# Performance work log

Measured on AMD Instinct MI355X. Metric: run time of the kernel, lower is better.

The kernel has to match this reference:

```python
import jax, jax.numpy as jnp
import numpy as np

B, N, E = 64, 512, 8192          # graphs, nodes per graph, edges per graph
F_IN, H, C = 128, 128, 10        # in features, hidden, classes
K1, K2 = 256, 128                # dense pool cluster counts: ceil(.5*N), ceil(.5*K1)
EPS = 1e-15


def setup_inputs():
    key = jax.random.key(0)
    keys = jax.random.split(key, 32)
    it = iter(keys)
    def w(shape, fan_in):
        return jax.random.normal(next(it), shape, jnp.float32) / np.sqrt(fan_in)
    x = jax.random.normal(next(it), (B * N, F_IN), jnp.float32)
    src_l = jax.random.randint(next(it), (B, E), 0, N)
    dst_l = jax.random.randint(next(it), (B, E), 0, N)
    off = (jnp.arange(B) * N)[:, None]
    src = (src_l + off).reshape(-1).astype(jnp.int32)
    dst = (dst_l + off).reshape(-1).astype(jnp.int32)
    return dict(
        x=x, src=src, dst=dst,
        conv0_wr=w((F_IN, H), F_IN), conv0_wroot=w((F_IN, H), F_IN), conv0_b=jnp.zeros((H,), jnp.float32),
        sconv2_wr=w((H, H), H), sconv2_wroot=w((H, H), H), sconv2_b=jnp.zeros((H,), jnp.float32),
        sconv3_wr=w((H, H), H), sconv3_wroot=w((H, H), H), sconv3_b=jnp.zeros((H,), jnp.float32),
        sage1_wr=w((H, H), H), sage1_wroot=w((H, H), H), sage1_b=jnp.zeros((H,), jnp.float32),
        sage2_wr=w((H, H), H), sage2_wroot=w((H, H), H), sage2_b=jnp.zeros((H,), jnp.float32),
        pool0_w=w((H, K1), H), pool0_b=jnp.zeros((K1,), jnp.float32),
        pool1_w=w((H, K2), H), pool1_b=jnp.zeros((K2,), jnp.float32),
        p1=w((H,), H), p2=w((H,), H), p3=w((H,), H),
        lin1_1_w=w((2 * H, H), 2 * H), lin1_1_b=jnp.zeros((H,), jnp.float32),
        lin1_w=w((H, H), H), lin1_b=jnp.zeros((H,), jnp.float32),
        lin2_w=w((2 * H, C), 2 * H), lin2_b=jnp.zeros((C,), jnp.float32),
    )


def _graph_conv(x, src, dst, emask, wr, wroot, b, n):
    # PyG GraphConv: lin_rel(sum_j x_j) + lin_root(x_i); invalid edges masked to 0.
    msg = x[src] * emask[:, None]
    agg = jax.ops.segment_sum(msg, dst, num_segments=n)
    return agg @ wr + x @ wroot + b


def _topk_pool(x, score_w, src, dst, emask, n_per_graph, k):
    # TopK pooling (MPoolS): score = x.w/||w||, keep top ratio*n per graph, gate by tanh(score).
    score = x @ score_w / (jnp.linalg.norm(score_w) + 1e-16)
    idx = jax.lax.top_k(score.reshape(B, n_per_graph), k)[1]
    perm = (idx + (jnp.arange(B) * n_per_graph)[:, None]).reshape(-1)
    new_x = x[perm] * jnp.tanh(score[perm])[:, None]
    new_id = jnp.full((B * n_per_graph,), -1, jnp.int32).at[perm].set(
        jnp.arange(B * k, dtype=jnp.int32))
    ns, nd = new_id[src], new_id[dst]
    valid = (ns >= 0) & (nd >= 0) & (emask > 0)
    return new_x, jnp.where(valid, ns, 0), jnp.where(valid, nd, 0), valid.astype(x.dtype)


def _readout(x, k):
    # gmp || gap per graph (nodes are contiguous, k per graph)
    xr = x.reshape(B, k, -1)
    return jnp.concatenate([xr.max(axis=1), xr.mean(axis=1)], axis=-1)


def _dense_sage(x, adj, wr, wroot, b):
    agg = (adj @ x) / jnp.clip(adj.sum(-1, keepdims=True), 1.0, None)
    return agg @ wr + x @ wroot + b


def _dense_mincut_pool(x, adj, s):
    s = jax.nn.softmax(s, axis=-1)
    k = s.shape[-1]
    out = jnp.einsum('bnk,bnf->bkf', s, x)
    out_adj = jnp.einsum('bnk,bnm,bml->bkl', s, adj, s)
    mincut_num = jnp.trace(out_adj, axis1=-2, axis2=-1)
    deg = adj.sum(-1)
    mincut_den = jnp.einsum('bn,bnk,bnk->b', deg, s, s)
    mc = -jnp.mean(mincut_num / (mincut_den + EPS))
    ss = jnp.einsum('bnk,bnl->bkl', s, s)
    ss_n = jnp.linalg.norm(ss, axis=(1, 2), keepdims=True)
    eye = jnp.eye(k, dtype=x.dtype)
    o = jnp.mean(jnp.linalg.norm(ss / (ss_n + EPS) - eye / jnp.sqrt(k), axis=(1, 2)))
    di = jnp.arange(k)
    out_adj = out_adj.at[:, di, di].set(0.0)
    dpool = jnp.sqrt(out_adj.sum(-1)) + EPS
    out_adj = out_adj / dpool[:, :, None] / dpool[:, None, :]
    return out, out_adj, mc, o


def _forward(x, src, dst, conv0_wr, conv0_wroot, conv0_b, sconv2_wr, sconv2_wroot, sconv2_b,
             sconv3_wr, sconv3_wroot, sconv3_b, sage1_wr, sage1_wroot, sage1_b,
             sage2_wr, sage2_wroot, sage2_b, pool0_w, pool0_b, pool1_w, pool1_b,
             p1, p2, p3, lin1_1_w, lin1_1_b, lin1_w, lin1_b, lin2_w, lin2_b):
    relu = jax.nn.relu
    e0 = jnp.ones((src.shape[0],), x.dtype)
    x0 = relu(_graph_conv(x, src, dst, e0, conv0_wr, conv0_wroot, conv0_b, B * N))
    # ---- sparse (MPoolS / top-k) branch, stage 1 ----
    sx, s1, d1, m1 = _topk_pool(x0, p1, src, dst, e0, N, N // 2)
    sx1 = _readout(sx, N // 2)
    # ---- dense (DiffPool-style) branch ----
    xd = x0.reshape(B, N, H)                               # to_dense_batch (full mask)
    g = src // N
    adj = jnp.zeros((B, N, N), x.dtype).at[g, src % N, dst % N].add(1.0)  # to_dense_adj
    s = xd @ pool0_w + pool0_b
    xd, adj, mc, o = _dense_mincut_pool(xd, adj, s)
    xd = relu(_dense_sage(xd, adj, sage1_wr, sage1_wroot, sage1_b))
    s = xd @ pool1_w + pool1_b
    xd, adj, mc2, o2 = _dense_mincut_pool(xd, adj, s)
    mc, o = mc + mc2, o + o2
    xd = _dense_sage(xd, adj, sage2_wr, sage2_wroot, sage2_b)
    xg = relu(xd.mean(axis=1) @ lin1_w + lin1_b)
    # ---- sparse branch, stages 2 and 3 ----
    sx = relu(_graph_conv(sx, s1, d1, m1, sconv2_wr, sconv2_wroot, sconv2_b, B * (N // 2)))
    sx, s2, d2, m2 = _topk_pool(sx, p2, s1, d1, m1, N // 2, N // 4)
    sx2 = _readout(sx, N // 4)
    sx = relu(_graph_conv(sx, s2, d2, m2, sconv3_wr, sconv3_wroot, sconv3_b, B * (N // 4)))
    sx, s3, d3, m3 = _topk_pool(sx, p3, s2, d2, m2, N // 4, N // 8)
    sx3 = _readout(sx, N // 8)
    sxr = relu((sx1 + sx2 + sx3) @ lin1_1_w + lin1_1_b)
    logits = jnp.concatenate([sxr, xg], axis=-1) @ lin2_w + lin2_b
    return logits, mc, o


def reference(x, src, dst, conv0_wr, conv0_wroot, conv0_b, sconv2_wr, sconv2_wroot, sconv2_b,
              sconv3_wr, sconv3_wroot, sconv3_b, sage1_wr, sage1_wroot, sage1_b,
              sage2_wr, sage2_wroot, sage2_b, pool0_w, pool0_b, pool1_w, pool1_b,
              p1, p2, p3, lin1_1_w, lin1_1_b, lin1_w, lin1_b, lin2_w, lin2_b):
    return _forward(x, src, dst, conv0_wr, conv0_wroot, conv0_b, sconv2_wr, sconv2_wroot,
                    sconv2_b, sconv3_wr, sconv3_wroot, sconv3_b, sage1_wr, sage1_wroot,
                    sage1_b, sage2_wr, sage2_wroot, sage2_b, pool0_w, pool0_b, pool1_w,
                    pool1_b, p1, p2, p3, lin1_1_w, lin1_1_b, lin1_w, lin1_b, lin2_w, lin2_b)
```

## Files before the change

kernel.cpp:

```cpp
#include <hip/hip_runtime.h>
#include <math.h>

#define NGRAPH 64
#define NE 524288
#define EPG 8192
#define TSZ 2560

typedef short s16x8 __attribute__((ext_vector_type(8)));
typedef float f32x4 __attribute__((ext_vector_type(4)));

__device__ inline unsigned short f2bf(float f) {
    unsigned int u = __float_as_uint(f);
    return (unsigned short)((u + 0x7FFFu + ((u >> 16) & 1u)) >> 16);
}

__global__ void edge_count(const int* __restrict__ key, const float* __restrict__ mask,
                           int* __restrict__ counts) {
    int e = blockIdx.x * 256 + threadIdx.x;
    if (e < NE && (!mask || mask[e] > 0.f)) atomicAdd(&counts[key[e]], 1);
}

__global__ __launch_bounds__(512) void scan_offsets(const int* __restrict__ counts,
        int* __restrict__ offs, int* __restrict__ cursor, int nPerGraph) {
    __shared__ int s[512];
    const int g = blockIdx.x, t = threadIdx.x;
    int v = (t < nPerGraph) ? counts[g * nPerGraph + t] : 0;
    s[t] = v; __syncthreads();
    for (int d = 1; d < 512; d <<= 1) {
        int u = (t >= d) ? s[t - d] : 0;
        __syncthreads();
        s[t] += u;
        __syncthreads();
    }
    if (t < nPerGraph) {
        int o = g * EPG + s[t] - v;
        offs[g * nPerGraph + t] = o;
        cursor[g * nPerGraph + t] = o;
    }
}

__global__ void edge_fill(const int* __restrict__ key, const int* __restrict__ payload,
                          const float* __restrict__ mask, int* __restrict__ cursor,
                          int* __restrict__ elist) {
    int e = blockIdx.x * 256 + threadIdx.x;
    if (e < NE && (!mask || mask[e] > 0.f)) {
        int p = atomicAdd(&cursor[key[e]], 1);
        elist[p] = payload[e];
    }
}

__global__ __launch_bounds__(256) void gather_csr(
    const float* __restrict__ xfeat, int Fx,
    const int* __restrict__ offs, const int* __restrict__ cnts,
    const int* __restrict__ elist,
    float* __restrict__ out, int totRows, int rowsPerGraph)
{
    const int gid = (blockIdx.x * 256 + threadIdx.x) >> 5;
    const int lane = threadIdx.x & 31;
    const int csh = (Fx == 256) ? 1 : 0;
    const int rid = gid >> csh;
    const int c0 = (gid & ((1 << csh) - 1)) << 7;
    if (rid >= totRows) return;
    const int row = (rid & 63) * rowsPerGraph + (rid >> 6);
    const int beg = offs[row];
    const int n = cnts[row];
    const long long co = (long long)c0 + (lane << 2);
    float4 acc = make_float4(0.f, 0.f, 0.f, 0.f);
    int j = 0;
    for (; j + 4 <= n; j += 4) {
        const int n0 = elist[beg + j], n1 = elist[beg + j + 1];
        const int n2 = elist[beg + j + 2], n3 = elist[beg + j + 3];
        const float4 v0 = *(const float4*)&xfeat[(long long)n0 * Fx + co];
        const float4 v1 = *(const float4*)&xfeat[(long long)n1 * Fx + co];
        const float4 v2 = *(const float4*)&xfeat[(long long)n2 * Fx + co];
        const float4 v3 = *(const float4*)&xfeat[(long long)n3 * Fx + co];
        acc.x += v0.x + v1.x + v2.x + v3.x;
        acc.y += v0.y + v1.y + v2.y + v3.y;
        acc.z += v0.z + v1.z + v2.z + v3.z;
        acc.w += v0.w + v1.w + v2.w + v3.w;
    }
    for (; j < n; ++j) {
        const float4 v = *(const float4*)&xfeat[(long long)elist[beg + j] * Fx + co];
        acc.x += v.x; acc.y += v.y; acc.z += v.z; acc.w += v.w;
    }
    *(float4*)&out[(long long)row * Fx + co] = acc;
}

__global__ void i2f(const int* __restrict__ a, float* __restrict__ b, int n) {
    int i = blockIdx.x * 256 + threadIdx.x;
    if (i < n) b[i] = (float)a[i];
}

__global__ void wconv2_t(const float* __restrict__ W1, const float* __restrict__ W2,
                         int K1, int K2, int Nn,
                         unsigned short* __restrict__ outh, unsigned short* __restrict__ outl) {
    int idx = blockIdx.x * 256 + threadIdx.x;
    int Kt = K1 + K2;
    if (idx >= Nn * Kt) return;
    int n = idx / Kt, k = idx - n * Kt;
    float v = (k < K1) ? W1[(long long)k * Nn + n] : W2[(long long)(k - K1) * Nn + n];
    unsigned short h = f2bf(v);
    float hf = __uint_as_float((unsigned int)h << 16);
    outh[idx] = h;
    outl[idx] = f2bf(v - hf);
}

__device__ inline void stageN_split(const float* __restrict__ src, int ldk, int k0,
                                    short* lds, int tid, const float* __restrict__ rs, int m0) {
    const int r = tid >> 2, kq = (tid & 3) << 3;
    const float* p = src + (long long)r * ldk + k0 + kq;
    float v[8];
    *(float4*)v = *(const float4*)p;
    *(float4*)(v + 4) = *(const float4*)(p + 4);
    if (rs) { float s = rs[m0 + r]; for (int i = 0; i < 8; ++i) v[i] *= s; }
    s16x8 hv, lv;
    #pragma unroll
    for (int i = 0; i < 8; ++i) {
        unsigned short h = f2bf(v[i]);
        float hf = __uint_as_float((unsigned int)h << 16);
        hv[i] = (short)h;
        lv[i] = (short)f2bf(v[i] - hf);
    }
    *(s16x8*)(lds + r * 40 + kq) = hv;
    *(s16x8*)(lds + TSZ + r * 40 + kq) = lv;
}

__device__ inline void stageT_split(const float* __restrict__ src, int ldm, int k0, int m0,
                                    short* lds, int tid) {
    const int kp = tid >> 4, mc = tid & 15;
    const int k = kp << 1;
    const float* p0 = src + (long long)(k0 + k) * ldm + m0 + mc;
    const float* p1 = p0 + ldm;
    #pragma unroll
    for (int i = 0; i < 4; ++i) {
        float a = p0[i << 4], b = p1[i << 4];
        unsigned short ha = f2bf(a), hb = f2bf(b);
        float hfa = __uint_as_float((unsigned int)ha << 16);
        float hfb = __uint_as_float((unsigned int)hb << 16);
        unsigned short la = f2bf(a - hfa), lb = f2bf(b - hfb);
        const int o = (mc + (i << 4)) * 40 + k;
        *(unsigned int*)(lds + o) = (unsigned int)ha | ((unsigned int)hb << 16);
        *(unsigned int*)(lds + o + TSZ) = (unsigned int)la | ((unsigned int)lb << 16);
    }
}

__device__ inline void stageW_split(const unsigned short* __restrict__ wh,
                                    const unsigned short* __restrict__ wl, int ldk,
                                    int n0, int k0, short* lds, int tid) {
    const int r = tid >> 2, kq = (tid & 3) << 3;
    *(s16x8*)(lds + r * 40 + kq) = *(const s16x8*)(wh + (long long)(n0 + r) * ldk + k0 + kq);
    *(s16x8*)(lds + TSZ + r * 40 + kq) = *(const s16x8*)(wl + (long long)(n0 + r) * ldk + k0 + kq);
}

__device__ inline void mfma_split(const short* As, const short* Bs, int wm, int wn,
                                  int l15, int quad, f32x4 (&acc)[2][2]) {
    const int ko = quad << 3;
    s16x8 ah[2], al[2], bh[2], bl[2];
    #pragma unroll
    for (int i = 0; i < 2; ++i) {
        const int ra = (wm + (i << 4) + l15) * 40 + ko;
        const int rb = (wn + (i << 4) + l15) * 40 + ko;
        ah[i] = *(const s16x8*)&As[ra];
        al[i] = *(const s16x8*)&As[TSZ + ra];
        bh[i] = *(const s16x8*)&Bs[rb];
        bl[i] = *(const s16x8*)&Bs[TSZ + rb];
    }
    #pragma unroll
    for (int mi = 0; mi < 2; ++mi)
    #pragma unroll
    for (int ni = 0; ni < 2; ++ni) {
        f32x4 c = acc[mi][ni];
        c = __builtin_amdgcn_mfma_f32_16x16x32_bf16(ah[mi], bh[ni], c, 0, 0, 0);
        c = __builtin_amdgcn_mfma_f32_16x16x32_bf16(ah[mi], bl[ni], c, 0, 0, 0);
        c = __builtin_amdgcn_mfma_f32_16x16x32_bf16(al[mi], bh[ni], c, 0, 0, 0);
        acc[mi][ni] = c;
    }
}

__global__ __launch_bounds__(256) void gemm_aw(
    const float* __restrict__ A1, int K1, const float* __restrict__ A2, int K2,
    const float* __restrict__ rscale,
    const unsigned short* __restrict__ Wh, const unsigned short* __restrict__ Wl,
    const float* __restrict__ bias, float* __restrict__ C, int Nn, int doRelu)
{
    __shared__ short As[2 * TSZ], Bs[2 * TSZ];
    const int m0 = blockIdx.y << 6, n0 = blockIdx.x << 6;
    const int tid = threadIdx.x, lane = tid & 63, wv = tid >> 6;
    const int l15 = lane & 15, quad = lane >> 4;
    const int wm = (wv & 1) << 5, wn = (wv >> 1) << 5;
    f32x4 acc[2][2] = {};
    const int Kt = K1 + K2;
    for (int k0 = 0; k0 < Kt; k0 += 32) {
        if (k0 < K1) stageN_split(A1 + (long long)m0 * K1, K1, k0, As, tid, rscale, m0);
        else         stageN_split(A2 + (long long)m0 * K2, K2, k0 - K1, As, tid, nullptr, 0);
        stageW_split(Wh, Wl, Kt, n0, k0, Bs, tid);
        __syncthreads();
        mfma_split(As, Bs, wm, wn, l15, quad, acc);
        __syncthreads();
    }
    #pragma unroll
    for (int mi = 0; mi < 2; ++mi)
    #pragma unroll
    for (int ni = 0; ni < 2; ++ni) {
        const int col = n0 + wn + (ni << 4) + l15;
        const float bv = bias ? bias[col] : 0.f;
        #pragma unroll
        for (int r = 0; r < 4; ++r) {
            const int row = m0 + wm + (mi << 4) + (quad << 2) + r;
            float v = acc[mi][ni][r] + bv;
            if (doRelu) v = fmaxf(v, 0.f);
            C[(long long)row * Nn + col] = v;
        }
    }
}

__global__ __launch_bounds__(256) void gemm_tt(
    const float* __restrict__ At, const float* __restrict__ Bkn,
    float* __restrict__ C, float* __restrict__ fro,
    int Kd, int Mm, int Nn, int dual,
    long long sA, long long sB, long long sC)
{
    __shared__ short As[2 * TSZ], Bs[2 * TSZ], A2s[2 * TSZ];
    __shared__ float redf[4];
    const int z = blockIdx.x;
    const float* Ap = At + (long long)z * sA;
    const float* Bp = Bkn + (long long)z * sB;
    const int m0 = blockIdx.y << 6, n0 = blockIdx.z << 6;
    const int tid = threadIdx.x, lane = tid & 63, wv = tid >> 6;
    const int l15 = lane & 15, quad = lane >> 4;
    const int wm = (wv & 1) << 5, wn = (wv >> 1) << 5;
    f32x4 acc[2][2] = {};
    f32x4 accA[2][2] = {};
    for (int k0 = 0; k0 < Kd; k0 += 32) {
        stageT_split(Ap, Mm, k0, m0, As, tid);
        stageT_split(Bp, Nn, k0, n0, Bs, tid);
        if (dual) stageT_split(Ap, Mm, k0, n0, A2s, tid);
        __syncthreads();
        mfma_split(As, Bs, wm, wn, l15, quad, acc);
        if (dual) mfma_split(As, A2s, wm, wn, l15, quad, accA);
        __syncthreads();
    }
    float* Cp = C + (long long)z * sC;
    #pragma unroll
    for (int mi = 0; mi < 2; ++mi)
    #pragma unroll
    for (int ni = 0; ni < 2; ++ni) {
        const int col = n0 + wn + (ni << 4) + l15;
        #pragma unroll
        for (int r = 0; r < 4; ++r) {
            const int row = m0 + wm + (mi << 4) + (quad << 2) + r;
            Cp[(long long)row * Nn + col] = acc[mi][ni][r];
        }
    }
    if (dual) {
        float s = 0.f;
        #pragma unroll
        for (int mi = 0; mi < 2; ++mi)
        #pragma unroll
        for (int ni = 0; ni < 2; ++ni)
        #pragma unroll
        for (int r = 0; r < 4; ++r) s += accA[mi][ni][r] * accA[mi][ni][r];
        for (int off = 32; off; off >>= 1) s += __shfl_xor(s, off);
        if (lane == 0) redf[wv] = s;
        __syncthreads();
        if (tid == 0) atomicAdd(&fro[z], redf[0] + redf[1] + redf[2] + redf[3]);
    }
}

__global__ __launch_bounds__(256) void gemm_nt(
    const float* __restrict__ A, const float* __restrict__ Bkn, float* __restrict__ C,
    int Kd, int Nn, long long sA, long long sB, long long sC)
{
    __shared__ short As[2 * TSZ], Bs[2 * TSZ];
    const int z = blockIdx.x;
    const int m0 = blockIdx.y << 6, n0 = blockIdx.z << 6;
    const float* Ap = A + (long long)z * sA + (long long)m0 * Kd;
    const float* Bp = Bkn + (long long)z * sB;
    const int tid = threadIdx.x, lane = tid & 63, wv = tid >> 6;
    const int l15 = lane & 15, quad = lane >> 4;
    const int wm = (wv & 1) << 5, wn = (wv >> 1) << 5;
    f32x4 acc[2][2] = {};
    for (int k0 = 0; k0 < Kd; k0 += 32) {
        stageN_split(Ap, Kd, k0, As, tid, nullptr, 0);
        stageT_split(Bp, Nn, k0, n0, Bs, tid);
        __syncthreads();
        mfma_split(As, Bs, wm, wn, l15, quad, acc);
        __syncthreads();
    }
    float* Cp = C + (long long)z * sC;
    #pragma unroll
    for (int mi = 0; mi < 2; ++mi)
    #pragma unroll
    for (int ni = 0; ni < 2; ++ni) {
        const int col = n0 + wn + (ni << 4) + l15;
        #pragma unroll
        for (int r = 0; r < 4; ++r) {
            const int row = m0 + wm + (mi << 4) + (quad << 2) + r;
            Cp[(long long)row * Nn + col] = acc[mi][ni][r];
        }
    }
}

__global__ __launch_bounds__(256) void softmax_rows_wave(
    float* __restrict__ sm, int L,
    const float* __restrict__ deg,
    float* __restrict__ rowq2, float* __restrict__ rowdq2, int totRows)
{
    const int wid = (blockIdx.x * 256 + threadIdx.x) >> 6;
    const int lane = threadIdx.x & 63;
    if (wid >= totRows) return;
    float* rowp = sm + (long long)wid * L;
    const int nv = L >> 6;
    float v[4];
    if (nv == 4) {
        float4 t = *(const float4*)&rowp[lane << 2];
        v[0] = t.x; v[1] = t.y; v[2] = t.z; v[3] = t.w;
    } else {
        float2 t = *(const float2*)&rowp[lane << 1];
        v[0] = t.x; v[1] = t.y;
    }
    float mx = v[0];
    for (int i = 1; i < nv; ++i) mx = fmaxf(mx, v[i]);
    for (int off = 32; off; off >>= 1) mx = fmaxf(mx, __shfl_xor(mx, off));
    float s = 0.f;
    for (int i = 0; i < nv; ++i) { v[i] = expf(v[i] - mx); s += v[i]; }
    for (int off = 32; off; off >>= 1) s += __shfl_xor(s, off);
    const float inv = 1.f / s;
    float q2 = 0.f;
    for (int i = 0; i < nv; ++i) { float p = v[i] * inv; v[i] = p; q2 += p * p; }
    if (nv == 4) *(float4*)&rowp[lane << 2] = make_float4(v[0], v[1], v[2], v[3]);
    else         *(float2*)&rowp[lane << 1] = make_float2(v[0], v[1]);
    for (int off = 32; off; off >>= 1) q2 += __shfl_xor(q2, off);
    if (lane == 0) { rowq2[wid] = q2; rowdq2[wid] = deg[wid] * q2; }
}

__global__ __launch_bounds__(256) void zdiag_rowsum_wave(
    float* __restrict__ adj, int K, float* __restrict__ dpool,
    float* __restrict__ rowdiag, int totRows)
{
    const int wid = (blockIdx.x * 256 + threadIdx.x) >> 6;
    const int lane = threadIdx.x & 63;
    if (wid >= totRows) return;
    const int b = wid / K;
    const int dcol = wid - b * K;
    float* rowp = adj + (long long)wid * K;
    const int nv = K >> 6;
    float s = 0.f, dval = 0.f;
    for (int q = 0; q < nv; ++q) {
        int c = lane + (q << 6);
        float v = rowp[c];
        if (c == dcol) { dval = v; rowp[c] = 0.f; v = 0.f; }
        s += v;
    }
    for (int off = 32; off; off >>= 1) s += __shfl_xor(s, off);
    if (lane == (dcol & 63)) rowdiag[wid] = dval;
    if (lane == 0) dpool[wid] = sqrtf(s) + 1e-15f;
}

__global__ __launch_bounds__(256) void norm_adj_wave(
    float* __restrict__ adj, int K, const float* __restrict__ dpool,
    float* __restrict__ rowsum, float* __restrict__ rscale, int totRows)
{
    const int wid = (blockIdx.x * 256 + threadIdx.x) >> 6;
    const int lane = threadIdx.x & 63;
    if (wid >= totRows) return;
    const int b = wid / K;
    float* rowp = adj + (long long)wid * K;
    const float inv_r = 1.f / dpool[wid];
    const int nv = K >> 6;
    float s = 0.f;
    for (int q = 0; q < nv; ++q) {
        int c = lane + (q << 6);
        float v = rowp[c] * inv_r / dpool[b * K + c];
        rowp[c] = v;
        s += v;
    }
    for (int off = 32; off; off >>= 1) s += __shfl_xor(s, off);
    if (lane == 0) { rowsum[wid] = s; rscale[wid] = 1.f / fmaxf(s, 1.f); }
}

__global__ __launch_bounds__(256) void reduce2_pergraph(
    const float* __restrict__ a, const float* __restrict__ b, int rowsPerGraph,
    float* __restrict__ outA, float* __restrict__ outB)
{
    __shared__ float redA[4], redB[4];
    const int g = blockIdx.x, t = threadIdx.x;
    float sa = 0.f, sb = 0.f;
    for (int i = t; i < rowsPerGraph; i += 256) {
        sa += a[g * rowsPerGraph + i];
        if (b) sb += b[g * rowsPerGraph + i];
    }
    for (int off = 32; off; off >>= 1) { sa += __shfl_xor(sa, off); sb += __shfl_xor(sb, off); }
    const int wv = t >> 6;
    if ((t & 63) == 0) { redA[wv] = sa; redB[wv] = sb; }
    __syncthreads();
    if (t == 0) {
        outA[g] = redA[0] + redA[1] + redA[2] + redA[3];
        if (outB) outB[g] = redB[0] + redB[1] + redB[2] + redB[3];
    }
}

__global__ void score_kernel(const float* __restrict__ x, const float* __restrict__ p,
                             float* __restrict__ score, int rows) {
    int wid = (blockIdx.x * blockDim.x + threadIdx.x) >> 6;
    int lane = threadIdx.x & 63;
    if (wid >= rows) return;
    float p0 = p[lane], p1 = p[64 + lane];
    float a = x[(long long)wid * 128 + lane] * p0
            + x[(long long)wid * 128 + 64 + lane] * p1;
    float b = p0 * p0 + p1 * p1;
    for (int off = 32; off; off >>= 1) { a += __shfl_down(a, off); b += __shfl_down(b, off); }
    if (lane == 0) score[wid] = a / (sqrtf(b) + 1e-16f);
}

__global__ void topk_kernel(const float* __restrict__ score, int n, int k,
                            int* __restrict__ new_id, int* __restrict__ sel,
                            float* __restrict__ gate) {
    __shared__ float sc[512];
    __shared__ int keep[512];
    int g = blockIdx.x, tid = threadIdx.x;
    for (int i = tid; i < n; i += 256) sc[i] = score[g * n + i];
    __syncthreads();
    for (int i = tid; i < n; i += 256) {
        float si = sc[i]; int rank = 0;
        for (int j = 0; j < n; j++) { float sj = sc[j]; rank += (sj > si) || (sj == si && j < i); }
        keep[i] = rank < k;
    }
    __syncthreads();
    for (int i = tid; i < n; i += 256) {
        if (keep[i]) {
            int pos = 0;
            for (int j = 0; j < i; j++) pos += keep[j];
            new_id[g * n + i] = g * k + pos;
            sel[g * k + pos] = g * n + i;
            gate[g * k + pos] = tanhf(sc[i]);
        } else new_id[g * n + i] = -1;
    }
}

__global__ void gather_gate(const float* __restrict__ x, const int* __restrict__ sel,
                            const float* __restrict__ gate, float* __restrict__ out, int rows) {
    int t = blockIdx.x * blockDim.x + threadIdx.x;
    int r = t >> 5, q = (t & 31) << 2;
    if (r >= rows) return;
    float4 v = *(const float4*)&x[(long long)sel[r] * 128 + q];
    float gt = gate[r];
    v.x *= gt; v.y *= gt; v.z *= gt; v.w *= gt;
    *(float4*)&out[(long long)r * 128 + q] = v;
}

__global__ void remap_edges_count(const int* __restrict__ s, const int* __restrict__ d,
                                  const float* __restrict__ m, const int* __restrict__ new_id,
                                  int* __restrict__ so, int* __restrict__ do_,
                                  float* __restrict__ mo, int* __restrict__ counts) {
    int e = blockIdx.x * blockDim.x + threadIdx.x;
    if (e >= NE) return;
    int ns = new_id[s[e]], nd = new_id[d[e]];
    bool v = (ns >= 0) && (nd >= 0) && (m ? (m[e] > 0.f) : true);
    so[e] = v ? ns : 0; do_[e] = v ? nd : 0; mo[e] = v ? 1.f : 0.f;
    if (v) atomicAdd(&counts[nd], 1);
}

__global__ void readout_part(const float* __restrict__ x, int k,
                             float* __restrict__ pmax, float* __restrict__ psum) {
    int g = blockIdx.x, seg = blockIdx.y, f = threadIdx.x;
    int per = k >> 2;
    int r0 = seg * per;
    float mx0 = -INFINITY, mx1 = -INFINITY, sm0 = 0.f, sm1 = 0.f;
    int r = r0;
    for (; r + 2 <= r0 + per; r += 2) {
        float v0 = x[(long long)(g * k + r) * 128 + f];
        float v1 = x[(long long)(g * k + r + 1) * 128 + f];
        mx0 = fmaxf(mx0, v0); sm0 += v0;
        mx1 = fmaxf(mx1, v1); sm1 += v1;
    }
    for (; r < r0 + per; ++r) { float v = x[(long long)(g * k + r) * 128 + f]; mx0 = fmaxf(mx0, v); sm0 += v; }
    pmax[(g * 4 + seg) * 128 + f] = fmaxf(mx0, mx1);
    psum[(g * 4 + seg) * 128 + f] = sm0 + sm1;
}

__global__ void readout_comb(const float* __restrict__ pmax, const float* __restrict__ psum,
                             int k, float* __restrict__ sxsum) {
    int g = blockIdx.x, f = threadIdx.x;
    float mx = -INFINITY, sm = 0.f;
    #pragma unroll
    for (int s = 0; s < 4; ++s) {
        mx = fmaxf(mx, pmax[(g * 4 + s) * 128 + f]);
        sm += psum[(g * 4 + s) * 128 + f];
    }
    sxsum[g * 256 + f] += mx;
    sxsum[g * 256 + 128 + f] += sm / k;
}

__global__ void mc_o_kernel(const float* __restrict__ acc, float sqrtk,
                            float* __restrict__ mcpart, float* __restrict__ opart) {
    int t = threadIdx.x;
    float numv = acc[t], denv = acc[64 + t], trv = acc[128 + t], frov = acc[192 + t];
    float mcb = numv / (denv + 1e-15f);
    float ssn = sqrtf(frov) + 1e-15f;
    float ob = sqrtf(fmaxf(frov / (ssn * ssn) - 2.f * trv / (ssn * sqrtk) + 1.f, 0.f));
    for (int off = 32; off; off >>= 1) { mcb += __shfl_down(mcb, off); ob += __shfl_down(ob, off); }
    if (t == 0) { mcpart[0] = -mcb / 64.f; opart[0] = ob / 64.f; }
}

__global__ void mean_lin(const float* __restrict__ xd, const float* __restrict__ W,
                         const float* __restrict__ bias, float* __restrict__ xg, int nNodes) {
    __shared__ float meanv[128];
    int b = blockIdx.x, t = threadIdx.x;
    float s = 0.f;
    for (int n = 0; n < nNodes; n++) s += xd[(long long)(b * nNodes + n) * 128 + t];
    meanv[t] = s / nNodes; __syncthreads();
    float acc = bias[t];
    for (int i = 0; i < 128; i++) acc += meanv[i] * W[i * 128 + t];
    xg[b * 128 + t] = fmaxf(acc, 0.f);
}

__global__ void final_head(const float* __restrict__ sxsum, const float* __restrict__ w11,
                           const float* __restrict__ b11, const float* __restrict__ xg,
                           const float* __restrict__ w2, const float* __restrict__ b2,
                           float* __restrict__ outLogits) {
    __shared__ float sin_[256];
    __shared__ float cat[256];
    int b = blockIdx.x, t = threadIdx.x;
    sin_[t] = sxsum[b * 256 + t];
    sin_[t + 128] = sxsum[b * 256 + 128 + t];
    __syncthreads();
    float acc = b11[t];
    for (int i = 0; i < 256; i++) acc += sin_[i] * w11[i * 128 + t];
    cat[t] = fmaxf(acc, 0.f);
    cat[128 + t] = xg[b * 128 + t];
    __syncthreads();
    if (t < 10) {
        float a = b2[t];
        for (int i = 0; i < 256; i++) a += cat[i] * w2[i * 10 + t];
        outLogits[b * 10 + t] = a;
    }
}

__global__ void write_scalars(const float* __restrict__ mcpart, const float* __restrict__ opart,
                              float* __restrict__ out) {
    if (threadIdx.x == 0) { out[640] = mcpart[0] + mcpart[1]; out[641] = opart[0] + opart[1]; }
}

extern "C" void kernel_launch(void* const* d_in, const int* in_sizes, int n_in,
                              void* d_out, int out_size, void* d_ws, size_t ws_size,
                              hipStream_t stream) {
    const float* x         = (const float*)d_in[0];
    const int*   src       = (const int*)d_in[1];
    const int*   dst       = (const int*)d_in[2];
    const float* conv0_wr  = (const float*)d_in[3];
    const float* conv0_wrt = (const float*)d_in[4];
    const float* conv0_b   = (const float*)d_in[5];
    const float* sc2_wr    = (const float*)d_in[6];
    const float* sc2_wrt   = (const float*)d_in[7];
    const float* sc2_b     = (const float*)d_in[8];
    const float* sc3_wr    = (const float*)d_in[9];
    const float* sc3_wrt   = (const float*)d_in[10];
    const float* sc3_b     = (const float*)d_in[11];
    const float* sg1_wr    = (const float*)d_in[12];
    const float* sg1_wrt   = (const float*)d_in[13];
    const float* sg1_b     = (const float*)d_in[14];
    const float* sg2_wr    = (const float*)d_in[15];
    const float* sg2_wrt   = (const float*)d_in[16];
    const float* sg2_b     = (const float*)d_in[17];
    const float* pool0_w   = (const float*)d_in[18];
    const float* pool0_b   = (const float*)d_in[19];
    const float* pool1_w   = (const float*)d_in[20];
    const float* pool1_b   = (const float*)d_in[21];
    const float* p1        = (const float*)d_in[22];
    const float* p2        = (const float*)d_in[23];
    const float* p3        = (const float*)d_in[24];
    const float* l11_w     = (const float*)d_in[25];
    const float* l11_b     = (const float*)d_in[26];
    const float* l1_w      = (const float*)d_in[27];
    const float* l1_b      = (const float*)d_in[28];
    const float* l2_w      = (const float*)d_in[29];
    const float* l2_b      = (const float*)d_in[30];
    float* out = (float*)d_out;

    char* w = (char*)d_ws;
    const unsigned long long MBy = 1ull << 20;
    float* x0    = (float*)(w + 0);
    float* BIG1  = (float*)(w + 16 * MBy);
    float* BIG2  = (float*)(w + 48 * MBy);
    float* agg   = (float*)(w + 80 * MBy);
    float* outx1 = (float*)(w + 96 * MBy);
    float* adj1  = (float*)(w + 104 * MBy);
    int*   s1    = (int*)(w + 120 * MBy);
    int*   d1    = (int*)(w + 122 * MBy);
    float* m1    = (float*)(w + 124 * MBy);
    int*   s2e   = (int*)(w + 126 * MBy);
    int*   d2e   = (int*)(w + 128 * MBy);
    float* m2e   = (float*)(w + 130 * MBy);
    char*  misc  = w + 132 * MBy;
    float* score = (float*)(misc);
    int*   sel   = (int*)(misc + 128 * 1024);
    float* gate  = (float*)(misc + 192 * 1024);
    int*   newid = (int*)(misc + 256 * 1024);
    float* deg   = (float*)(misc + 384 * 1024);
    float* dpool = (float*)(misc + 512 * 1024);
    float* rowsum2 = (float*)(misc + 576 * 1024);
    float* rscale2 = (float*)(misc + 640 * 1024);
    float* dpool2  = (float*)(misc + 704 * 1024);
    float* rowsum3 = (float*)(misc + 736 * 1024);
    float* rscale3 = (float*)(misc + 768 * 1024);
    float* accs    = (float*)(misc + 800 * 1024);
    float* mcpart  = accs + 512;
    float* opart   = accs + 514;
    float* sxsum   = (float*)(misc + 900 * 1024);
    float* xg      = (float*)(misc + 964 * 1024);

    unsigned short* wt_sg1h   = (unsigned short*)(misc + 1024 * 1024);
    unsigned short* wt_sg1l   = wt_sg1h + 32768;
    unsigned short* wt_sg2h   = wt_sg1l + 32768;
    unsigned short* wt_sg2l   = wt_sg2h + 32768;
    unsigned short* wt_pool0h = wt_sg2l + 32768;
    unsigned short* wt_pool0l = wt_pool0h + 32768;
    unsigned short* wt_pool1h = wt_pool0l + 32768;
    unsigned short* wt_pool1l = wt_pool1h + 32768;
    unsigned short* wt_c0h    = wt_pool1l + 32768;
    unsigned short* wt_c0l    = wt_c0h + 32768;
    unsigned short* wt_sc2h   = wt_c0l + 32768;
    unsigned short* wt_sc2l   = wt_sc2h + 32768;
    unsigned short* wt_sc3h   = wt_sc2l + 32768;
    unsigned short* wt_sc3l   = wt_sc3h + 32768;

    float* pmax = (float*)(misc + 2048 * 1024);
    float* psum = pmax + 32768;

    float* rowq2  = score;
    float* rowdq2 = (float*)newid;
    float* rowdiag = (float*)sel;

    float* s_sm  = BIG1;
    float* Tbuf  = BIG2;
    float* xd1   = BIG2;
    float* AX    = BIG2 + 2 * 1024 * 1024;
    float* s2sm  = BIG2 + 4 * 1024 * 1024;
    float* T2    = BIG2 + 6 * 1024 * 1024;
    float* outx2 = BIG1;
    float* adj2b = BIG1 + 1024 * 1024;
    float* xd2   = BIG1 + 2 * 1024 * 1024;
    float* sxA   = BIG1 + 3 * 1024 * 1024;
    float* sxE   = BIG1 + 5 * 1024 * 1024;
    float* sxB   = x0;
    float* sxC   = x0 + 2 * 1024 * 1024;
    float* sxD   = x0 + 3 * 1024 * 1024;

    char* adjc = (char*)adj1;
    int* elA  = (int*)(adjc + 0);
    int* elB  = (int*)(adjc + 2 * MBy);
    int* cntA = (int*)(adjc + 4 * MBy);
    int* offA = (int*)(adjc + 4 * MBy + 256 * 1024);
    int* curA = (int*)(adjc + 4 * MBy + 512 * 1024);
    int* cntB = (int*)(adjc + 4 * MBy + 768 * 1024);
    int* offB = (int*)(adjc + 5 * MBy);
    int* curB = (int*)(adjc + 5 * MBy + 256 * 1024);
    char* aggc = (char*)agg;
    int* elC  = (int*)(aggc + 8 * MBy);
    int* elD  = (int*)(aggc + 10 * MBy);
    int* cntC = (int*)(aggc + 12 * MBy);
    int* offC = (int*)(aggc + 12 * MBy + 256 * 1024);
    int* curC = (int*)(aggc + 12 * MBy + 512 * 1024);
    int* cntD = (int*)(aggc + 13 * MBy);
    int* offD = (int*)(aggc + 13 * MBy + 256 * 1024);
    int* curD = (int*)(aggc + 13 * MBy + 512 * 1024);

    hipMemsetAsync(accs, 0, 520 * sizeof(float), stream);
    hipMemsetAsync(sxsum, 0, 16384 * sizeof(float), stream);
    hipMemsetAsync(cntA, 0, 32768 * sizeof(int), stream);
    hipMemsetAsync(cntB, 0, 32768 * sizeof(int), stream);

    wconv2_t<<<128, 256, 0, stream>>>(sg1_wr, sg1_wrt, 128, 128, 128, wt_sg1h, wt_sg1l);
    wconv2_t<<<128, 256, 0, stream>>>(sg2_wr, sg2_wrt, 128, 128, 128, wt_sg2h, wt_sg2l);
    wconv2_t<<<128, 256, 0, stream>>>(pool0_w, nullptr, 128, 0, 256, wt_pool0h, wt_pool0l);
    wconv2_t<<<64, 256, 0, stream>>>(pool1_w, nullptr, 128, 0, 128, wt_pool1h, wt_pool1l);
    wconv2_t<<<128, 256, 0, stream>>>(conv0_wr, conv0_wrt, 128, 128, 128, wt_c0h, wt_c0l);
    wconv2_t<<<128, 256, 0, stream>>>(sc2_wr, sc2_wrt, 128, 128, 128, wt_sc2h, wt_sc2l);
    wconv2_t<<<128, 256, 0, stream>>>(sc3_wr, sc3_wrt, 128, 128, 128, wt_sc3h, wt_sc3l);

    edge_count<<<2048, 256, 0, stream>>>(dst, nullptr, cntA);
    edge_count<<<2048, 256, 0, stream>>>(src, nullptr, cntB);
    scan_offsets<<<64, 512, 0, stream>>>(cntA, offA, curA, 512);
    scan_offsets<<<64, 512, 0, stream>>>(cntB, offB, curB, 512);
    edge_fill<<<2048, 256, 0, stream>>>(dst, src, nullptr, curA, elA);
    edge_fill<<<2048, 256, 0, stream>>>(src, dst, nullptr, curB, elB);

    gather_csr<<<4096, 256, 0, stream>>>(x, 128, offA, cntA, elA, agg, 32768, 512);
    gemm_aw<<<dim3(2, 512), 256, 0, stream>>>(agg, 128, x, 128, nullptr, wt_c0h, wt_c0l,
        conv0_b, x0, 128, 1);

    i2f<<<128, 256, 0, stream>>>(cntB, deg, 32768);
    gemm_aw<<<dim3(4, 512), 256, 0, stream>>>(x0, 128, nullptr, 0, nullptr, wt_pool0h, wt_pool0l,
        pool0_b, s_sm, 256, 0);
    softmax_rows_wave<<<8192, 256, 0, stream>>>(s_sm, 256, deg, rowq2, rowdq2, 32768);
    reduce2_pergraph<<<64, 256, 0, stream>>>(rowq2, rowdq2, 512, accs + 128, accs + 64);
    gather_csr<<<8192, 256, 0, stream>>>(s_sm, 256, offB, cntB, elB, Tbuf, 32768, 512);
    gemm_tt<<<dim3(64, 4, 2), 256, 0, stream>>>(s_sm, x0, outx1, nullptr, 512, 256, 128, 0,
        512 * 256, 512 * 128, 256 * 128);
    gemm_tt<<<dim3(64, 4, 4), 256, 0, stream>>>(s_sm, Tbuf, adj1, accs + 192, 512, 256, 256, 1,
        512 * 256, 512 * 256, 256 * 256);
    zdiag_rowsum_wave<<<4096, 256, 0, stream>>>(adj1, 256, dpool, rowdiag, 16384);
    reduce2_pergraph<<<64, 256, 0, stream>>>(rowdiag, nullptr, 256, accs + 0, nullptr);
    norm_adj_wave<<<4096, 256, 0, stream>>>(adj1, 256, dpool, rowsum2, rscale2, 16384);
    mc_o_kernel<<<1, 64, 0, stream>>>(accs, 16.f, mcpart, opart);
    gemm_nt<<<dim3(64, 4, 2), 256, 0, stream>>>(adj1, outx1, AX, 256, 128,
        256 * 256, 256 * 128, 256 * 128);
    gemm_aw<<<dim3(2, 256), 256, 0, stream>>>(AX, 128, outx1, 128, rscale2, wt_sg1h, wt_sg1l,
        sg1_b, xd1, 128, 1);
    gemm_aw<<<dim3(2, 256), 256, 0, stream>>>(xd1, 128, nullptr, 0, nullptr, wt_pool1h, wt_pool1l,
        pool1_b, s2sm, 128, 0);
    softmax_rows_wave<<<4096, 256, 0, stream>>>(s2sm, 128, rowsum2, rowq2, rowdq2, 16384);
    reduce2_pergraph<<<64, 256, 0, stream>>>(rowq2, rowdq2, 256, accs + 384, accs + 320);
    gemm_nt<<<dim3(64, 4, 2), 256, 0, stream>>>(adj1, s2sm, T2, 256, 128,
        256 * 256, 256 * 128, 256 * 128);
    gemm_tt<<<dim3(64, 2, 2), 256, 0, stream>>>(s2sm, xd1, outx2, nullptr, 256, 128, 128, 0,
        256 * 128, 256 * 128, 128 * 128);
    gemm_tt<<<dim3(64, 2, 2), 256, 0, stream>>>(s2sm, T2, adj2b, accs + 448, 256, 128, 128, 1,
        256 * 128, 256 * 128, 128 * 128);
    zdiag_rowsum_wave<<<2048, 256, 0, stream>>>(adj2b, 128, dpool2, rowdiag, 8192);
    reduce2_pergraph<<<64, 256, 0, stream>>>(rowdiag, nullptr, 128, accs + 256, nullptr);
    norm_adj_wave<<<2048, 256, 0, stream>>>(adj2b, 128, dpool2, rowsum3, rscale3, 8192);
    mc_o_kernel<<<1, 64, 0, stream>>>(accs + 256, sqrtf(128.f), mcpart + 1, opart + 1);
    gemm_nt<<<dim3(64, 2, 2), 256, 0, stream>>>(adj2b, outx2, AX, 128, 128,
        128 * 128, 128 * 128, 128 * 128);
    gemm_aw<<<dim3(2, 128), 256, 0, stream>>>(AX, 128, outx2, 128, rscale3, wt_sg2h, wt_sg2l,
        sg2_b, xd2, 128, 0);
    mean_lin<<<64, 128, 0, stream>>>(xd2, l1_w, l1_b, xg, 128);

    score_kernel<<<8192, 256, 0, stream>>>(x0, p1, score, 32768);
    topk_kernel<<<64, 256, 0, stream>>>(score, 512, 256, newid, sel, gate);
    gather_gate<<<2048, 256, 0, stream>>>(x0, sel, gate, sxA, 16384);
    hipMemsetAsync(cntC, 0, 16384 * sizeof(int), stream);
    remap_edges_count<<<2048, 256, 0, stream>>>(src, dst, nullptr, newid, s1, d1, m1, cntC);
    readout_part<<<dim3(64, 4), 128, 0, stream>>>(sxA, 256, pmax, psum);
    readout_comb<<<64, 128, 0, stream>>>(pmax, psum, 256, sxsum);
    scan_offsets<<<64, 512, 0, stream>>>(cntC, offC, curC, 256);
    edge_fill<<<2048, 256, 0, stream>>>(d1, s1, m1, curC, elC);
    gather_csr<<<2048, 256, 0, stream>>>(sxA, 128, offC, cntC, elC, agg, 16384, 256);
    gemm_aw<<<dim3(2, 256), 256, 0, stream>>>(agg, 128, sxA, 128, nullptr, wt_sc2h, wt_sc2l,
        sc2_b, sxB, 128, 1);
    score_kernel<<<4096, 256, 0, stream>>>(sxB, p2, score, 16384);
    topk_kernel<<<64, 256, 0, stream>>>(score, 256, 128, newid, sel, gate);
    gather_gate<<<1024, 256, 0, stream>>>(sxB, sel, gate, sxC, 8192);
    hipMemsetAsync(cntD, 0, 8192 * sizeof(int), stream);
    remap_edges_count<<<2048, 256, 0, stream>>>(s1, d1, m1, newid, s2e, d2e, m2e, cntD);
    readout_part<<<dim3(64, 4), 128, 0, stream>>>(sxC, 128, pmax, psum);
    readout_comb<<<64, 128, 0, stream>>>(pmax, psum, 128, sxsum);
    scan_offsets<<<64, 512, 0, stream>>>(cntD, offD, curD, 128);
    edge_fill<<<2048, 256, 0, stream>>>(d2e, s2e, m2e, curD, elD);
    gather_csr<<<1024, 256, 0, stream>>>(sxC, 128, offD, cntD, elD, agg, 8192, 128);
    gemm_aw<<<dim3(2, 128), 256, 0, stream>>>(agg, 128, sxC, 128, nullptr, wt_sc3h, wt_sc3l,
        sc3_b, sxD, 128, 1);
    score_kernel<<<2048, 256, 0, stream>>>(sxD, p3, score, 8192);
    topk_kernel<<<64, 256, 0, stream>>>(score, 128, 64, newid, sel, gate);
    gather_gate<<<512, 256, 0, stream>>>(sxD, sel, gate, sxE, 4096);
    readout_part<<<dim3(64, 4), 128, 0, stream>>>(sxE, 64, pmax, psum);
    readout_comb<<<64, 128, 0, stream>>>(pmax, psum, 64, sxsum);

    final_head<<<64, 128, 0, stream>>>(sxsum, l11_w, l11_b, xg, l2_w, l2_b, out);
    write_scalars<<<1, 1, 0, stream>>>(mcpart, opart, out);
}
```

Before: 713.9 us.

## Fuse small launches and exploit symmetry in dual Gram GEMM

Merges the seven weight-conversion launches into one kernel and folds the int-to-float degree conversion into scan_offsets. It also fuses score computation into topk_kernel and merges the mc/o scalar kernels and write_scalars into a single launch. The dual Gram-norm path in gemm_tt now computes only upper-triangular tiles, weighting off-diagonal tiles by two, using high-part-only bf16 staging and MFMA. Fewer launches cut dispatch overhead, but the fused topk does a serial 128-wide dot product per thread on only 64 blocks, and the hi-only Frobenius term loses some precision.

```diff
diff --git a/kernel.cpp b/kernel.cpp
--- a/kernel.cpp
+++ b/kernel.cpp
@@ -21,7 +21,8 @@
 }
 
 __global__ __launch_bounds__(512) void scan_offsets(const int* __restrict__ counts,
-        int* __restrict__ offs, int* __restrict__ cursor, int nPerGraph) {
+        int* __restrict__ offs, int* __restrict__ cursor, int nPerGraph,
+        float* __restrict__ degOut) {
     __shared__ int s[512];
     const int g = blockIdx.x, t = threadIdx.x;
     int v = (t < nPerGraph) ? counts[g * nPerGraph + t] : 0;
@@ -36,6 +37,7 @@
         int o = g * EPG + s[t] - v;
         offs[g * nPerGraph + t] = o;
         cursor[g * nPerGraph + t] = o;
+        if (degOut) degOut[g * nPerGraph + t] = (float)v;
     }
 }
 
@@ -86,23 +88,26 @@
     *(float4*)&out[(long long)row * Fx + co] = acc;
 }
 
-__global__ void i2f(const int* __restrict__ a, float* __restrict__ b, int n) {
-    int i = blockIdx.x * 256 + threadIdx.x;
-    if (i < n) b[i] = (float)a[i];
-}
-
-__global__ void wconv2_t(const float* __restrict__ W1, const float* __restrict__ W2,
-                         int K1, int K2, int Nn,
-                         unsigned short* __restrict__ outh, unsigned short* __restrict__ outl) {
+struct WSpec {
+    const float* w1; const float* w2; int K1; int K2; int Nn;
+    unsigned short* oh; unsigned short* ol;
+};
+
+__global__ void wconv_all(WSpec s0, WSpec s1, WSpec s2, WSpec s3, WSpec s4, WSpec s5, WSpec s6) {
+    WSpec s;
+    switch (blockIdx.y) {
+        case 0: s = s0; break; case 1: s = s1; break; case 2: s = s2; break;
+        case 3: s = s3; break; case 4: s = s4; break; case 5: s = s5; break;
+        default: s = s6; break;
+    }
     int idx = blockIdx.x * 256 + threadIdx.x;
-    int Kt = K1 + K2;
-    if (idx >= Nn * Kt) return;
+    int Kt = s.K1 + s.K2;
+    if (idx >= s.Nn * Kt) return;
     int n = idx / Kt, k = idx - n * Kt;
-    float v = (k < K1) ? W1[(long long)k * Nn + n] : W2[(long long)(k - K1) * Nn + n];
+    float v = (k < s.K1) ? s.w1[(long long)k * s.Nn + n] : s.w2[(long long)(k - s.K1) * s.Nn + n];
     unsigned short h = f2bf(v);
-    float hf = __uint_as_float((unsigned int)h << 16);
-    outh[idx] = h;
-    outl[idx] = f2bf(v - hf);
+    s.oh[idx] = h;
+    s.ol[idx] = f2bf(v - __uint_as_float((unsigned int)h << 16));
 }
 
 __device__ inline void stageN_split(const float* __restrict__ src, int ldk, int k0,
@@ -144,6 +149,20 @@
     }
 }
 
+__device__ inline void stageT_hi(const float* __restrict__ src, int ldm, int k0, int m0,
+                                 short* lds, int tid) {
+    const int kp = tid >> 4, mc = tid & 15;
+    const int k = kp << 1;
+    const float* p0 = src + (long long)(k0 + k) * ldm + m0 + mc;
+    const float* p1 = p0 + ldm;
+    #pragma unroll
+    for (int i = 0; i < 4; ++i) {
+        unsigned short ha = f2bf(p0[i << 4]), hb = f2bf(p1[i << 4]);
+        *(unsigned int*)(lds + (mc + (i << 4)) * 40 + k) =
+            (unsigned int)ha | ((unsigned int)hb << 16);
+    }
+}
+
 __device__ inline void stageW_split(const unsigned short* __restrict__ wh,
                                     const unsigned short* __restrict__ wl, int ldk,
                                     int n0, int k0, short* lds, int tid) {
@@ -175,6 +194,22 @@
         c = __builtin_amdgcn_mfma_f32_16x16x32_bf16(al[mi], bh[ni], c, 0, 0, 0);
         acc[mi][ni] = c;
     }
+}
+
+__device__ inline void mfma_hi(const short* As, const short* Bs, int wm, int wn,
+                               int l15, int quad, f32x4 (&acc)[2][2]) {
+    const int ko = quad << 3;
+    s16x8 ah[2], bh[2];
+    #pragma unroll
+    for (int i = 0; i < 2; ++i) {
+        ah[i] = *(const s16x8*)&As[(wm + (i << 4) + l15) * 40 + ko];
+        bh[i] = *(const s16x8*)&Bs[(wn + (i << 4) + l15) * 40 + ko];
+    }
+    #pragma unroll
+    for (int mi = 0; mi < 2; ++mi)
+    #pragma unroll
+    for (int ni = 0; ni < 2; ++ni)
+        acc[mi][ni] = __builtin_amdgcn_mfma_f32_16x16x32_bf16(ah[mi], bh[ni], acc[mi][ni], 0, 0, 0);
 }
 
 __global__ __launch_bounds__(256) void gemm_aw(
@@ -220,7 +255,7 @@
     int Kd, int Mm, int Nn, int dual,
     long long sA, long long sB, long long sC)
 {
-    __shared__ short As[2 * TSZ], Bs[2 * TSZ], A2s[2 * TSZ];
+    __shared__ short As[2 * TSZ], Bs[2 * TSZ], A2s[TSZ];
     __shared__ float redf[4];
     const int z = blockIdx.x;
     const float* Ap = At + (long long)z * sA;
@@ -229,15 +264,16 @@
     const int tid = threadIdx.x, lane = tid & 63, wv = tid >> 6;
     const int l15 = lane & 15, quad = lane >> 4;
     const int wm = (wv & 1) << 5, wn = (wv >> 1) << 5;
+    const int fw = dual ? ((m0 < n0) ? 2 : ((m0 == n0) ? 1 : 0)) : 0;
     f32x4 acc[2][2] = {};
     f32x4 accA[2][2] = {};
     for (int k0 = 0; k0 < Kd; k0 += 32) {
         stageT_split(Ap, Mm, k0, m0, As, tid);
         stageT_split(Bp, Nn, k0, n0, Bs, tid);
-        if (dual) stageT_split(Ap, Mm, k0, n0, A2s, tid);
+        if (fw) stageT_hi(Ap, Mm, k0, n0, A2s, tid);
         __syncthreads();
         mfma_split(As, Bs, wm, wn, l15, quad, acc);
-        if (dual) mfma_split(As, A2s, wm, wn, l15, quad, accA);
+        if (fw) mfma_hi(As, A2s, wm, wn, l15, quad, accA);
         __syncthreads();
     }
     float* Cp = C + (long long)z * sC;
@@ -252,7 +288,7 @@
             Cp[(long long)row * Nn + col] = acc[mi][ni][r];
         }
     }
-    if (dual) {
+    if (fw) {
         float s = 0.f;
         #pragma unroll
         for (int mi = 0; mi < 2; ++mi)
@@ -260,6 +296,7 @@
         for (int ni = 0; ni < 2; ++ni)
         #pragma unroll
         for (int r = 0; r < 4; ++r) s += accA[mi][ni][r] * accA[mi][ni][r];
+        s *= (float)fw;
         for (int off = 32; off; off >>= 1) s += __shfl_xor(s, off);
         if (lane == 0) redf[wv] = s;
         __syncthreads();
@@ -400,26 +437,29 @@
     }
 }
 
-__global__ void score_kernel(const float* __restrict__ x, const float* __restrict__ p,
-                             float* __restrict__ score, int rows) {
-    int wid = (blockIdx.x * blockDim.x + threadIdx.x) >> 6;
-    int lane = threadIdx.x & 63;
-    if (wid >= rows) return;
-    float p0 = p[lane], p1 = p[64 + lane];
-    float a = x[(long long)wid * 128 + lane] * p0
-            + x[(long long)wid * 128 + 64 + lane] * p1;
-    float b = p0 * p0 + p1 * p1;
-    for (int off = 32; off; off >>= 1) { a += __shfl_down(a, off); b += __shfl_down(b, off); }
-    if (lane == 0) score[wid] = a / (sqrtf(b) + 1e-16f);
-}
-
-__global__ void topk_kernel(const float* __restrict__ score, int n, int k,
+__global__ void topk_kernel(const float* __restrict__ x, const float* __restrict__ p,
+                            int n, int k,
                             int* __restrict__ new_id, int* __restrict__ sel,
                             float* __restrict__ gate) {
     __shared__ float sc[512];
     __shared__ int keep[512];
     int g = blockIdx.x, tid = threadIdx.x;
-    for (int i = tid; i < n; i += 256) sc[i] = score[g * n + i];
+    float pn2 = 0.f;
+    for (int f = 0; f < 128; f += 4) {
+        float4 pv = *(const float4*)&p[f];
+        pn2 += pv.x * pv.x + pv.y * pv.y + pv.z * pv.z + pv.w * pv.w;
+    }
+    const float inv = 1.f / (sqrtf(pn2) + 1e-16f);
+    for (int i = tid; i < n; i += 256) {
+        const float* xr = x + (long long)(g * n + i) * 128;
+        float d = 0.f;
+        for (int f = 0; f < 128; f += 4) {
+            float4 v = *(const float4*)&xr[f];
+            float4 pv = *(const float4*)&p[f];
+            d += v.x * pv.x + v.y * pv.y + v.z * pv.z + v.w * pv.w;
+        }
+        sc[i] = d * inv;
+    }
     __syncthreads();
     for (int i = tid; i < n; i += 256) {
         float si = sc[i]; int rank = 0;
@@ -492,15 +532,23 @@
     sxsum[g * 256 + 128 + f] += sm / k;
 }
 
-__global__ void mc_o_kernel(const float* __restrict__ acc, float sqrtk,
-                            float* __restrict__ mcpart, float* __restrict__ opart) {
+__global__ void mc_o_write(const float* __restrict__ accs, float* __restrict__ out) {
+    __shared__ float rm[2], ro[2];
     int t = threadIdx.x;
-    float numv = acc[t], denv = acc[64 + t], trv = acc[128 + t], frov = acc[192 + t];
+    int wvi = t >> 6, lane = t & 63;
+    const float* acc = accs + wvi * 256;
+    float sqrtk = wvi ? sqrtf(128.f) : 16.f;
+    float numv = acc[lane], denv = acc[64 + lane], trv = acc[128 + lane], frov = acc[192 + lane];
     float mcb = numv / (denv + 1e-15f);
     float ssn = sqrtf(frov) + 1e-15f;
     float ob = sqrtf(fmaxf(frov / (ssn * ssn) - 2.f * trv / (ssn * sqrtk) + 1.f, 0.f));
     for (int off = 32; off; off >>= 1) { mcb += __shfl_down(mcb, off); ob += __shfl_down(ob, off); }
-    if (t == 0) { mcpart[0] = -mcb / 64.f; opart[0] = ob / 64.f; }
+    if (lane == 0) { rm[wvi] = mcb; ro[wvi] = ob; }
+    __syncthreads();
+    if (t == 0) {
+        out[640] = -(rm[0] + rm[1]) / 64.f;
+        out[641] = (ro[0] + ro[1]) / 64.f;
+    }
 }
 
 __global__ void mean_lin(const float* __restrict__ xd, const float* __restrict__ W,
@@ -535,11 +583,6 @@
         for (int i = 0; i < 256; i++) a += cat[i] * w2[i * 10 + t];
         outLogits[b * 10 + t] = a;
     }
-}
-
-__global__ void write_scalars(const float* __restrict__ mcpart, const float* __restrict__ opart,
-                              float* __restrict__ out) {
-    if (threadIdx.x == 0) { out[640] = mcpart[0] + mcpart[1]; out[641] = opart[0] + opart[1]; }
 }
 
 extern "C" void kernel_launch(void* const* d_in, const int* in_sizes, int n_in,
@@ -605,8 +648,6 @@
     float* rowsum3 = (float*)(misc + 736 * 1024);
     float* rscale3 = (float*)(misc + 768 * 1024);
     float* accs    = (float*)(misc + 800 * 1024);
-    float* mcpart  = accs + 512;
-    float* opart   = accs + 514;
     float* sxsum   = (float*)(misc + 900 * 1024);
     float* xg      = (float*)(misc + 964 * 1024);
 
@@ -671,18 +712,21 @@
     hipMemsetAsync(cntA, 0, 32768 * sizeof(int), stream);
     hipMemsetAsync(cntB, 0, 32768 * sizeof(int), stream);
 
-    wconv2_t<<<128, 256, 0, stream>>>(sg1_wr, sg1_wrt, 128, 128, 128, wt_sg1h, wt_sg1l);
-    wconv2_t<<<128, 256, 0, stream>>>(sg2_wr, sg2_wrt, 128, 128, 128, wt_sg2h, wt_sg2l);
-    wconv2_t<<<128, 256, 0, stream>>>(pool0_w, nullptr, 128, 0, 256, wt_pool0h, wt_pool0l);
-    wconv2_t<<<64, 256, 0, stream>>>(pool1_w, nullptr, 128, 0, 128, wt_pool1h, wt_pool1l);
-    wconv2_t<<<128, 256, 0, stream>>>(conv0_wr, conv0_wrt, 128, 128, 128, wt_c0h, wt_c0l);
-    wconv2_t<<<128, 256, 0, stream>>>(sc2_wr, sc2_wrt, 128, 128, 128, wt_sc2h, wt_sc2l);
-    wconv2_t<<<128, 256, 0, stream>>>(sc3_wr, sc3_wrt, 128, 128, 128, wt_sc3h, wt_sc3l);
+    {
+        WSpec a{sg1_wr, sg1_wrt, 128, 128, 128, wt_sg1h, wt_sg1l};
+        WSpec b{sg2_wr, sg2_wrt, 128, 128, 128, wt_sg2h, wt_sg2l};
+        WSpec c{pool0_w, nullptr, 128, 0, 256, wt_pool0h, wt_pool0l};
+        WSpec d{pool1_w, nullptr, 128, 0, 128, wt_pool1h, wt_pool1l};
+        WSpec e{conv0_wr, conv0_wrt, 128, 128, 128, wt_c0h, wt_c0l};
+        WSpec f{sc2_wr, sc2_wrt, 128, 128, 128, wt_sc2h, wt_sc2l};
+        WSpec g{sc3_wr, sc3_wrt, 128, 128, 128, wt_sc3h, wt_sc3l};
+        wconv_all<<<dim3(128, 7), 256, 0, stream>>>(a, b, c, d, e, f, g);
+    }
 
     edge_count<<<2048, 256, 0, stream>>>(dst, nullptr, cntA);
     edge_count<<<2048, 256, 0, stream>>>(src, nullptr, cntB);
-    scan_offsets<<<64, 512, 0, stream>>>(cntA, offA, curA, 512);
-    scan_offsets<<<64, 512, 0, stream>>>(cntB, offB, curB, 512);
+    scan_offsets<<<64, 512, 0, stream>>>(cntA, offA, curA, 512, nullptr);
+    scan_offsets<<<64, 512, 0, stream>>>(cntB, offB, curB, 512, deg);
     edge_fill<<<2048, 256, 0, stream>>>(dst, src, nullptr, curA, elA);
     edge_fill<<<2048, 256, 0, stream>>>(src, dst, nullptr, curB, elB);
 
@@ -690,7 +734,6 @@
     gemm_aw<<<dim3(2, 512), 256, 0, stream>>>(agg, 128, x, 128, nullptr, wt_c0h, wt_c0l,
         conv0_b, x0, 128, 1);
 
-    i2f<<<128, 256, 0, stream>>>(cntB, deg, 32768);
     gemm_aw<<<dim3(4, 512), 256, 0, stream>>>(x0, 128, nullptr, 0, nullptr, wt_pool0h, wt_pool0l,
         pool0_b, s_sm, 256, 0);
     softmax_rows_wave<<<8192, 256, 0, stream>>>(s_sm, 256, deg, rowq2, rowdq2, 32768);
@@ -703,7 +746,6 @@
     zdiag_rowsum_wave<<<4096, 256, 0, stream>>>(adj1, 256, dpool, rowdiag, 16384);
     reduce2_pergraph<<<64, 256, 0, stream>>>(rowdiag, nullptr, 256, accs + 0, nullptr);
     norm_adj_wave<<<4096, 256, 0, stream>>>(adj1, 256, dpool, rowsum2, rscale2, 16384);
-    mc_o_kernel<<<1, 64, 0, stream>>>(accs, 16.f, mcpart, opart);
     gemm_nt<<<dim3(64, 4, 2), 256, 0, stream>>>(adj1, outx1, AX, 256, 128,
         256 * 256, 256 * 128, 256 * 128);
     gemm_aw<<<dim3(2, 256), 256, 0, stream>>>(AX, 128, outx1, 128, rscale2, wt_sg1h, wt_sg1l,
@@ -721,43 +763,39 @@
     zdiag_rowsum_wave<<<2048, 256, 0, stream>>>(adj2b, 128, dpool2, rowdiag, 8192);
     reduce2_pergraph<<<64, 256, 0, stream>>>(rowdiag, nullptr, 128, accs + 256, nullptr);
     norm_adj_wave<<<2048, 256, 0, stream>>>(adj2b, 128, dpool2, rowsum3, rscale3, 8192);
-    mc_o_kernel<<<1, 64, 0, stream>>>(accs + 256, sqrtf(128.f), mcpart + 1, opart + 1);
     gemm_nt<<<dim3(64, 2, 2), 256, 0, stream>>>(adj2b, outx2, AX, 128, 128,
         128 * 128, 128 * 128, 128 * 128);
     gemm_aw<<<dim3(2, 128), 256, 0, stream>>>(AX, 128, outx2, 128, rscale3, wt_sg2h, wt_sg2l,
         sg2_b, xd2, 128, 0);
     mean_lin<<<64, 128, 0, stream>>>(xd2, l1_w, l1_b, xg, 128);
-
-    score_kernel<<<8192, 256, 0, stream>>>(x0, p1, score, 32768);
-    topk_kernel<<<64, 256, 0, stream>>>(score, 512, 256, newid, sel, gate);
+    mc_o_write<<<1, 128, 0, stream>>>(accs, out);
+
+    topk_kernel<<<64, 256, 0, stream>>>(x0, p1, 512, 256, newid, sel, gate);
     gather_gate<<<2048, 256, 0, stream>>>(x0, sel, gate, sxA, 16384);
     hipMemsetAsync(cntC, 0, 16384 * sizeof(int), stream);
     remap_edges_count<<<2048, 256, 0, stream>>>(src, dst, nullptr, newid, s1, d1, m1, cntC);
     readout_part<<<dim3(64, 4), 128, 0, stream>>>(sxA, 256, pmax, psum);
     readout_comb<<<64, 128, 0, stream>>>(pmax, psum, 256, sxsum);
-    scan_offsets<<<64, 512, 0, stream>>>(cntC, offC, curC, 256);
+    scan_offsets<<<64, 512, 0, stream>>>(cntC, offC, curC, 256, nullptr);
     edge_fill<<<2048, 256, 0, stream>>>(d1, s1, m1, curC, elC);
     gather_csr<<<2048, 256, 0, stream>>>(sxA, 128, offC, cntC, elC, agg, 16384, 256);
     gemm_aw<<<dim3(2, 256), 256, 0, stream>>>(agg, 128, sxA, 128, nullptr, wt_sc2h, wt_sc2l,
         sc2_b, sxB, 128, 1);
-    score_kernel<<<4096, 256, 0, stream>>>(sxB, p2, score, 16384);
-    topk_kernel<<<64, 256, 0, stream>>>(score, 256, 128, newid, sel, gate);
+    topk_kernel<<<64, 256, 0, stream>>>(sxB, p2, 256, 128, newid, sel, gate);
     gather_gate<<<1024, 256, 0, stream>>>(sxB, sel, gate, sxC, 8192);
     hipMemsetAsync(cntD, 0, 8192 * sizeof(int), stream);
     remap_edges_count<<<2048, 256, 0, stream>>>(s1, d1, m1, newid, s2e, d2e, m2e, cntD);
     readout_part<<<dim3(64, 4), 128, 0, stream>>>(sxC, 128, pmax, psum);
     readout_comb<<<64, 128, 0, stream>>>(pmax, psum, 128, sxsum);
-    scan_offsets<<<64, 512, 0, stream>>>(cntD, offD, curD, 128);
+    scan_offsets<<<64, 512, 0, stream>>>(cntD, offD, curD, 128, nullptr);
     edge_fill<<<2048, 256, 0, stream>>>(d2e, s2e, m2e, curD, elD);
     gather_csr<<<1024, 256, 0, stream>>>(sxC, 128, offD, cntD, elD, agg, 8192, 128);
     gemm_aw<<<dim3(2, 128), 256, 0, stream>>>(agg, 128, sxC, 128, nullptr, wt_sc3h, wt_sc3l,
         sc3_b, sxD, 128, 1);
-    score_kernel<<<2048, 256, 0, stream>>>(sxD, p3, score, 8192);
-    topk_kernel<<<64, 256, 0, stream>>>(score, 128, 64, newid, sel, gate);
+    topk_kernel<<<64, 256, 0, stream>>>(sxD, p3, 128, 64, newid, sel, gate);
     gather_gate<<<512, 256, 0, stream>>>(sxD, sel, gate, sxE, 4096);
     readout_part<<<dim3(64, 4), 128, 0, stream>>>(sxE, 64, pmax, psum);
     readout_comb<<<64, 128, 0, stream>>>(pmax, psum, 64, sxsum);
 
     final_head<<<64, 128, 0, stream>>>(sxsum, l11_w, l11_b, xg, l2_w, l2_b, out);
-    write_scalars<<<1, 1, 0, stream>>>(mcpart, opart, out);
-}
+}
```

New measurement: 685.5 us. 4.0% less time.
